# Kernel optimization log

Hardware: AMD Instinct MI355X
Metric: run time of the kernel (lower is better)

The kernel has to match this reference:

```python
import jax, jax.numpy as jnp
import numpy as np

# Model dims (from ModelArgs defaults)
B, S, DIM = 1, 1024, 2880
H, HKV, HD = 64, 8, 64        # query heads, kv heads, head dim
GROUP = H // HKV              # 8 query heads per kv head
WINDOW = 128                  # sliding window (layer_idx=0 -> active)
THETA = 150000.0


def setup_inputs() -> dict:
    key = jax.random.key(0)
    ks = jax.random.split(key, 10)
    rn = lambda k, shape, sc: (jax.random.normal(k, shape, jnp.float32) * sc)
    return {
        "x": rn(ks[0], (B, S, DIM), 1.0),
        "wq_w": rn(ks[1], (H * HD, DIM), 0.02),
        "wq_b": rn(ks[2], (H * HD,), 0.02),
        "wk_w": rn(ks[3], (HKV * HD, DIM), 0.02),
        "wk_b": rn(ks[4], (HKV * HD,), 0.02),
        "wv_w": rn(ks[5], (HKV * HD, DIM), 0.02),
        "wv_b": rn(ks[6], (HKV * HD,), 0.02),
        "wo_w": rn(ks[7], (DIM, H * HD), 0.02),
        "wo_b": rn(ks[8], (DIM,), 0.02),
        "sinks": rn(ks[9], (H,), 1.0),
    }


def _rope(t):
    # t: [B, S, h, HD]; half-split (rotate_half) RoPE with base THETA
    half = HD // 2
    inv_freq = 1.0 / (THETA ** (jnp.arange(half, dtype=jnp.float32) * 2.0 / HD))
    ang = jnp.arange(S, dtype=jnp.float32)[:, None] * inv_freq      # [S, half]
    cos = jnp.cos(ang)[None, :, None, :]
    sin = jnp.sin(ang)[None, :, None, :]
    t1, t2 = t[..., :half], t[..., half:]
    return jnp.concatenate([t1 * cos - t2 * sin, t1 * sin + t2 * cos], axis=-1)


def reference(x, wq_w, wq_b, wk_w, wk_b, wv_w, wv_b, wo_w, wo_b, sinks):
    # Projections (nn.Linear: y = x @ W^T + b)
    q = (jnp.einsum('bsd,ed->bse', x, wq_w) + wq_b).reshape(B, S, H, HD)
    k = (jnp.einsum('bsd,ed->bse', x, wk_w) + wk_b).reshape(B, S, HKV, HD)
    v = (jnp.einsum('bsd,ed->bse', x, wv_w) + wv_b).reshape(B, S, HKV, HD)

    q = _rope(q)
    k = _rope(k)

    # GQA: expand kv heads to match query heads
    k = jnp.repeat(k, GROUP, axis=2)   # [B, S, H, HD]
    v = jnp.repeat(v, GROUP, axis=2)

    scale = HD ** -0.5
    scores = jnp.einsum('bihd,bjhd->bhij', q, k) * scale   # [B, H, S, S]

    # Causal + sliding-window mask: attend to j with 0 <= i-j < WINDOW
    i = jnp.arange(S)[:, None]
    j = jnp.arange(S)[None, :]
    allowed = (j <= i) & ((i - j) < WINDOW)
    scores = jnp.where(allowed, scores, jnp.float32(-1e30))

    # Softmax with per-head learnable sink logit folded into normalization
    sink = sinks[None, :, None, None]                       # [1, H, 1, 1]
    m = jnp.maximum(jnp.max(scores, axis=-1, keepdims=True), sink)
    e = jnp.exp(scores - m)
    denom = jnp.sum(e, axis=-1, keepdims=True) + jnp.exp(sink - m)
    probs = e / denom                                       # sink mass dropped

    out = jnp.einsum('bhij,bjhd->bihd', probs, v).reshape(B, S, H * HD)
    return jnp.einsum('bse,de->bsd', out, wo_w) + wo_b
```

## Files before the change

kernel.cpp:

```cpp
#include <hip/hip_runtime.h>

typedef __attribute__((ext_vector_type(4))) float f32x4;
typedef __attribute__((ext_vector_type(8))) short s16x8;
typedef unsigned short u16;

#define DEVI __device__ __forceinline__

DEVI u16 f2bf(float f) {
    union { float f; unsigned int u; } v; v.f = f;
    unsigned int r = v.u + 0x7FFFu + ((v.u >> 16) & 1u);
    return (u16)(r >> 16);
}
DEVI float bf2f(u16 b) {
    union { unsigned int u; float f; } v; v.u = ((unsigned int)b) << 16;
    return v.f;
}

typedef __attribute__((address_space(1))) void gv_t;
typedef __attribute__((address_space(3))) void sv_t;

#define GLOAD16(SRC, DST) __builtin_amdgcn_global_load_lds( \
    (gv_t*)(SRC), (sv_t*)(DST), 16, 0, 0)

DEVI f32x4 mfma_bf16(s16x8 a, s16x8 b, f32x4 c) {
    return __builtin_amdgcn_mfma_f32_16x16x32_bf16(a, b, c, 0, 0, 0);
}

template<bool AF32>
__global__ __launch_bounds__(512, 4) void gemmrs(
    const void* __restrict__ Ap, int lda, int kit, int ntot,
    const float* __restrict__ W0, int t0, int n0, int c0,
    const float* __restrict__ W1, int t1, int n1, int c1,
    const float* __restrict__ W2, int t2, int n2, int c2,
    u16* __restrict__ C, int ldc, long long cstride)
{
    __shared__ u16 Als[2][128 * 64];
    __shared__ u16 Bls[2][128 * 64];

    const int lin = blockIdx.x;
    const int xc  = lin & 7;
    const int mm  = lin >> 3;
    const int nbl = xc + 8 * (mm >> 3);
    const int yt  = mm & 7;
    if (nbl >= ntot) return;

    const float* Af = (const float*)Ap;
    const u16*   Ab = (const u16*)Ap;

    const int tid  = threadIdx.x;
    const int lane = tid & 63;
    const int wid  = tid >> 6;
    const int li   = lane & 15;
    const int lg   = lane >> 4;
    const int m0   = yt * 128;

    const float* W; int nt0, nsz, cb;
    if (nbl < t0)           { W = W0; nt0 = nbl * 128;             nsz = n0; cb = c0; }
    else if (nbl < t0 + t1) { W = W1; nt0 = (nbl - t0) * 128;      nsz = n1; cb = c1; }
    else                    { W = W2; nt0 = (nbl - t0 - t1) * 128; nsz = n2; cb = c2; }

    const int z  = blockIdx.z;
    const int S  = gridDim.z;
    const int it0 = (z * kit) / S;
    const int it1 = ((z + 1) * kit) / S;
    u16* Cp = C + (long long)z * cstride;

    const int wm = (wid >> 2) * 64;
    const int wn = (wid & 3) * 32;

    const int srow = tid >> 3;
    const int c8   = tid & 7;
    const int sc   = c8 ^ (srow & 7);
    const int wrow0 = (nt0 + srow      > nsz - 1) ? nsz - 1 : nt0 + srow;
    const int wrow1 = (nt0 + srow + 64 > nsz - 1) ? nsz - 1 : nt0 + srow + 64;

    f32x4 acc[4][2];
    #pragma unroll
    for (int mi = 0; mi < 4; ++mi)
        #pragma unroll
        for (int ni = 0; ni < 2; ++ni)
            acc[mi][ni] = (f32x4){0.f, 0.f, 0.f, 0.f};

    f32x4 ra[2][2];
    s16x8 rab[2];
    f32x4 rw[2][2];

#define LOADT(TT)                                                               \
    do {                                                                        \
        int k0_ = (TT) * 64;                                                    \
        _Pragma("unroll")                                                       \
        for (int j = 0; j < 2; ++j) {                                           \
            int row_ = j * 64 + srow;                                           \
            if (AF32) {                                                         \
                const float* p_ = Af + (size_t)(m0 + row_) * lda + k0_ + c8 * 8;\
                ra[j][0] = *(const f32x4*)p_;                                   \
                ra[j][1] = *(const f32x4*)(p_ + 4);                             \
            } else {                                                            \
                rab[j] = *(const s16x8*)(Ab + (size_t)(m0 + row_) * lda + k0_ + c8 * 8); \
            }                                                                   \
            int wr_ = j ? wrow1 : wrow0;                                        \
            const float* q_ = W + (size_t)wr_ * lda + k0_ + c8 * 8;             \
            rw[j][0] = *(const f32x4*)q_;                                       \
            rw[j][1] = *(const f32x4*)(q_ + 4);                                 \
        }                                                                       \
    } while (0)

#define WRITET(BI)                                                              \
    do {                                                                        \
        _Pragma("unroll")                                                       \
        for (int j = 0; j < 2; ++j) {                                           \
            int row_ = j * 64 + srow;                                           \
            s16x8 va_;                                                          \
            if (AF32) {                                                         \
                _Pragma("unroll")                                               \
                for (int e = 0; e < 4; ++e) {                                   \
                    va_[e]     = (short)f2bf(ra[j][0][e]);                      \
                    va_[4 + e] = (short)f2bf(ra[j][1][e]);                      \
                }                                                               \
            } else {                                                            \
                va_ = rab[j];                                                   \
            }                                                                   \
            *(s16x8*)&Als[BI][row_ * 64 + sc * 8] = va_;                        \
            s16x8 vw_;                                                          \
            _Pragma("unroll")                                                   \
            for (int e = 0; e < 4; ++e) {                                       \
                vw_[e]     = (short)f2bf(rw[j][0][e]);                          \
                vw_[4 + e] = (short)f2bf(rw[j][1][e]);                          \
            }                                                                   \
            *(s16x8*)&Bls[BI][row_ * 64 + sc * 8] = vw_;                        \
        }                                                                       \
    } while (0)

    LOADT(it0);
    WRITET(0);
    __syncthreads();

    for (int t = it0; t < it1; ++t) {
        const int bi = (t - it0) & 1;

        if (t + 1 < it1) LOADT(t + 1);

        s16x8 bfv[2][2];
        #pragma unroll
        for (int ni = 0; ni < 2; ++ni)
            #pragma unroll
            for (int kc = 0; kc < 2; ++kc) {
                int row = wn + ni * 16 + li;
                int ch  = (kc * 4 + lg) ^ (row & 7);
                bfv[ni][kc] = *(const s16x8*)&Bls[bi][row * 64 + ch * 8];
            }
        #pragma unroll
        for (int mi = 0; mi < 4; ++mi) {
            s16x8 af[2];
            #pragma unroll
            for (int kc = 0; kc < 2; ++kc) {
                int row = wm + mi * 16 + li;
                int ch  = (kc * 4 + lg) ^ (row & 7);
                af[kc] = *(const s16x8*)&Als[bi][row * 64 + ch * 8];
            }
            #pragma unroll
            for (int ni = 0; ni < 2; ++ni)
                #pragma unroll
                for (int kc = 0; kc < 2; ++kc)
                    acc[mi][ni] = mfma_bf16(af[kc], bfv[ni][kc], acc[mi][ni]);
        }

        if (t + 1 < it1) WRITET(bi ^ 1);

        __syncthreads();
    }
#undef LOADT
#undef WRITET

    #pragma unroll
    for (int ni = 0; ni < 2; ++ni) {
        int colr = nt0 + wn + ni * 16 + li;
        if (colr < nsz) {
            #pragma unroll
            for (int mi = 0; mi < 4; ++mi)
                #pragma unroll
                for (int r = 0; r < 4; ++r) {
                    int row = m0 + wm + mi * 16 + lg * 4 + r;
                    Cp[(size_t)row * ldc + cb + colr] = f2bf(acc[mi][ni][r]);
                }
        }
    }
}

__global__ void rope_kernel(const u16* __restrict__ qkvp,
                            const float* __restrict__ qb, const float* __restrict__ kb,
                            const float* __restrict__ vb,
                            u16* __restrict__ qo, u16* __restrict__ ko, u16* __restrict__ vo)
{
    const long long PST = 1024LL * 5120;
    int id = blockIdx.x * 256 + threadIdx.x;
    int s  = id / 2560;
    int r  = id % 2560;
    const u16* r0 = qkvp + (size_t)s * 5120;
    if (r < 2304) {
        bool isq = r < 2048;
        int rr   = isq ? r : r - 2048;
        int hh   = rr >> 5;
        int d    = rr & 31;
        int col  = (isq ? 0 : 4096) + hh * 64 + d;
        int bcol = isq ? col : col - 4096;
        const float* bias = isq ? qb : kb;
        float t1 = bf2f(r0[col])      + bf2f(r0[col + PST])      + bf2f(r0[col + 2 * PST])      + bias[bcol];
        float t2 = bf2f(r0[col + 32]) + bf2f(r0[col + 32 + PST]) + bf2f(r0[col + 32 + 2 * PST]) + bias[bcol + 32];
        float ang = (float)s * exp2f((float)d * -0.5373314f);
        float sn, cs;
        sincosf(ang, &sn, &cs);
        float sc = isq ? 0.125f : 1.0f;
        float o1 = (t1 * cs - t2 * sn) * sc;
        float o2 = (t1 * sn + t2 * cs) * sc;
        u16* dst = isq ? qo : ko;
        int ldd  = isq ? 4096 : 512;
        dst[(size_t)s * ldd + bcol]      = f2bf(o1);
        dst[(size_t)s * ldd + bcol + 32] = f2bf(o2);
    } else {
        int e = (r - 2304) * 2;
        int c0 = 4608 + e;
        float v0 = bf2f(r0[c0])     + bf2f(r0[c0 + PST])     + bf2f(r0[c0 + 2 * PST])     + vb[e];
        float v1 = bf2f(r0[c0 + 1]) + bf2f(r0[c0 + 1 + PST]) + bf2f(r0[c0 + 1 + 2 * PST]) + vb[e + 1];
        vo[(size_t)s * 512 + e]     = f2bf(v0);
        vo[(size_t)s * 512 + e + 1] = f2bf(v1);
    }
}

__global__ void reduce_out_kernel(const u16* __restrict__ parts,
                                  const float* __restrict__ bias,
                                  float* __restrict__ out)
{
    int id = blockIdx.x * 256 + threadIdx.x;
    const long long stride = 1024LL * 2880;
    long long base = (long long)id * 8;
    float s[8];
    #pragma unroll
    for (int j = 0; j < 8; ++j) s[j] = 0.f;
    #pragma unroll
    for (int p = 0; p < 5; ++p) {
        s16x8 v = *(const s16x8*)(parts + p * stride + base);
        #pragma unroll
        for (int j = 0; j < 8; ++j) s[j] += bf2f((u16)v[j]);
    }
    int cb = (int)(base % 2880);
    f32x4 b0 = *(const f32x4*)(bias + cb);
    f32x4 b1 = *(const f32x4*)(bias + cb + 4);
    f32x4 o0 = {s[0] + b0[0], s[1] + b0[1], s[2] + b0[2], s[3] + b0[3]};
    f32x4 o1 = {s[4] + b1[0], s[5] + b1[1], s[6] + b1[2], s[7] + b1[3]};
    *(f32x4*)(out + base)     = o0;
    *(f32x4*)(out + base + 4) = o1;
}

__global__ __launch_bounds__(256, 2) void attn_kernel(
    const u16* __restrict__ Q, const u16* __restrict__ Kb, const u16* __restrict__ Vb,
    const float* __restrict__ sinks, u16* __restrict__ Ob)
{
    __shared__ u16 Kls[64 * 64];
    __shared__ u16 Pls[4][16 * 72];

    const int h    = blockIdx.x;
    const int qblk = blockIdx.y;
    const int kvh  = h >> 3;
    const int tid  = threadIdx.x;
    const int lane = tid & 63;
    const int w    = tid >> 6;
    const int li   = lane & 15;
    const int lg   = lane >> 4;
    const int qw   = qblk * 64 + w * 16;

    s16x8 aq[2];
    {
        const u16* qrow = Q + ((size_t)(qw + li) * 64 + h) * 64 + lg * 8;
        aq[0] = *(const s16x8*)(qrow);
        aq[1] = *(const s16x8*)(qrow + 32);
    }

    const float snk = sinks[h];
    float m_run[4], l_run[4];
    f32x4 oacc[4];
    #pragma unroll
    for (int r = 0; r < 4; ++r) { m_run[r] = snk; l_run[r] = 1.0f; }
    #pragma unroll
    for (int ni = 0; ni < 4; ++ni) oacc[ni] = (f32x4){0.f, 0.f, 0.f, 0.f};

    const int srow = tid >> 3;
    const int slc  = (tid & 7) ^ (srow & 7);

    for (int t = 0; t < 3; ++t) {
        int jt = qblk - 2 + t;
        if (jt < 0) continue;
        int j0 = jt * 64;

        #pragma unroll
        for (int it = 0; it < 2; ++it) {
            const u16* src = Kb + ((size_t)(j0 + it * 32 + srow) * 8 + kvh) * 64 + slc * 8;
            GLOAD16(src, &Kls[(it * 256 + w * 64) * 8]);
        }
        __syncthreads();

        f32x4 sc[4];
        #pragma unroll
        for (int nf = 0; nf < 4; ++nf) {
            sc[nf] = (f32x4){0.f, 0.f, 0.f, 0.f};
            #pragma unroll
            for (int kc = 0; kc < 2; ++kc) {
                int row = nf * 16 + li;
                int ch  = (kc * 4 + lg) ^ (row & 7);
                s16x8 bk = *(const s16x8*)&Kls[row * 64 + ch * 8];
                sc[nf] = mfma_bf16(aq[kc], bk, sc[nf]);
            }
        }

        #pragma unroll
        for (int r = 0; r < 4; ++r) {
            const int qg = qw + lg * 4 + r;
            float mx = -1e30f;
            #pragma unroll
            for (int nf = 0; nf < 4; ++nf) {
                int jg = j0 + nf * 16 + li;
                bool ok = (jg <= qg) && (qg - jg < 128);
                float v = ok ? sc[nf][r] : -1e30f;
                sc[nf][r] = v;
                mx = fmaxf(mx, v);
            }
            #pragma unroll
            for (int off = 1; off < 16; off <<= 1)
                mx = fmaxf(mx, __shfl_xor(mx, off));
            float mnew = fmaxf(m_run[r], mx);
            float corr = __expf(m_run[r] - mnew);
            m_run[r] = mnew;
            float rs = 0.f;
            #pragma unroll
            for (int nf = 0; nf < 4; ++nf) {
                float p = __expf(sc[nf][r] - mnew);
                rs += p;
                Pls[w][(lg * 4 + r) * 72 + nf * 16 + li] = f2bf(p);
            }
            #pragma unroll
            for (int off = 1; off < 16; off <<= 1)
                rs += __shfl_xor(rs, off);
            l_run[r] = l_run[r] * corr + rs;
            #pragma unroll
            for (int ni = 0; ni < 4; ++ni) oacc[ni][r] *= corr;
        }
        __syncthreads();

        #pragma unroll
        for (int kc = 0; kc < 2; ++kc) {
            s16x8 pa = *(const s16x8*)&Pls[w][li * 72 + kc * 32 + lg * 8];
            #pragma unroll
            for (int ni = 0; ni < 4; ++ni) {
                const u16* vsrc = Vb + ((size_t)(j0 + kc * 32 + lg * 8) * 8 + kvh) * 64 + ni * 16 + li;
                s16x8 bv;
                #pragma unroll
                for (int i = 0; i < 8; ++i) bv[i] = (short)vsrc[(size_t)i * 512];
                oacc[ni] = mfma_bf16(pa, bv, oacc[ni]);
            }
        }
    }

    #pragma unroll
    for (int r = 0; r < 4; ++r) {
        float inv = 1.0f / l_run[r];
        #pragma unroll
        for (int ni = 0; ni < 4; ++ni)
            Ob[((size_t)(qw + lg * 4 + r) * 64 + h) * 64 + ni * 16 + li] = f2bf(oacc[ni][r] * inv);
    }
}

extern "C" void kernel_launch(void* const* d_in, const int* in_sizes, int n_in,
                              void* d_out, int out_size, void* d_ws, size_t ws_size,
                              hipStream_t stream)
{
    const float* x     = (const float*)d_in[0];
    const float* wq_w  = (const float*)d_in[1];
    const float* wq_b  = (const float*)d_in[2];
    const float* wk_w  = (const float*)d_in[3];
    const float* wk_b  = (const float*)d_in[4];
    const float* wv_w  = (const float*)d_in[5];
    const float* wv_b  = (const float*)d_in[6];
    const float* wo_w  = (const float*)d_in[7];
    const float* wo_b  = (const float*)d_in[8];
    const float* sinks = (const float*)d_in[9];

    char* ws = (char*)d_ws;
    u16*   qkvp = (u16*)(ws + 35389440ULL);
    u16*   qr   = (u16*)(ws + 0);
    u16*   kr   = (u16*)(ws + 8388608ULL);
    u16*   vbf  = (u16*)(ws + 9437184ULL);
    u16*   attb = (u16*)(ws + 10485760ULL);
    u16*   oprt = (u16*)(ws + 58982400ULL);

    (void)in_sizes; (void)n_in; (void)out_size; (void)ws_size;

    gemmrs<true><<<dim3(320, 1, 3), 512, 0, stream>>>(x, 2880, 45, 40,
        wq_w, 32, 4096, 0,
        wk_w, 4, 512, 4096,
        wv_w, 4, 512, 4608,
        qkvp, 5120, 1024LL * 5120);
    rope_kernel<<<10240, 256, 0, stream>>>(qkvp, wq_b, wk_b, wv_b, qr, kr, vbf);
    attn_kernel<<<dim3(64, 16), 256, 0, stream>>>(qr, kr, vbf, sinks, attb);
    gemmrs<false><<<dim3(192, 1, 5), 512, 0, stream>>>(attb, 4096, 64, 23,
        wo_w, 23, 2880, 0,
        wo_w, 0, 0, 0,
        wo_w, 0, 0, 0,
        oprt, 2880, 1024LL * 2880);
    reduce_out_kernel<<<1440, 256, 0, stream>>>(oprt, wo_b, (float*)d_out);
}
```

Measured before the change: 141.1 us.

## Pre-convert x to bf16, load A tiles via global_load_lds, vectorize rope

```diff
diff --git a/kernel.cpp b/kernel.cpp
--- a/kernel.cpp
+++ b/kernel.cpp
@@ -26,9 +26,18 @@
     return __builtin_amdgcn_mfma_f32_16x16x32_bf16(a, b, c, 0, 0, 0);
 }
 
-template<bool AF32>
-__global__ __launch_bounds__(512, 4) void gemmrs(
-    const void* __restrict__ Ap, int lda, int kit, int ntot,
+__global__ void cvt_x_kernel(const float* __restrict__ x, u16* __restrict__ xb)
+{
+    int id = blockIdx.x * 256 + threadIdx.x;
+    f32x4 v = *(const f32x4*)(x + (size_t)id * 4);
+    union { u16 u[4]; unsigned long long ll; } o;
+    #pragma unroll
+    for (int j = 0; j < 4; ++j) o.u[j] = f2bf(v[j]);
+    *(unsigned long long*)(xb + (size_t)id * 4) = o.ll;
+}
+
+__global__ __launch_bounds__(512, 4) void gemmhy(
+    const u16* __restrict__ A, int lda, int kit, int ntot,
     const float* __restrict__ W0, int t0, int n0, int c0,
     const float* __restrict__ W1, int t1, int n1, int c1,
     const float* __restrict__ W2, int t2, int n2, int c2,
@@ -44,9 +53,6 @@
     const int yt  = mm & 7;
     if (nbl >= ntot) return;
 
-    const float* Af = (const float*)Ap;
-    const u16*   Ab = (const u16*)Ap;
-
     const int tid  = threadIdx.x;
     const int lane = tid & 63;
     const int wid  = tid >> 6;
@@ -68,12 +74,6 @@
     const int wm = (wid >> 2) * 64;
     const int wn = (wid & 3) * 32;
 
-    const int srow = tid >> 3;
-    const int c8   = tid & 7;
-    const int sc   = c8 ^ (srow & 7);
-    const int wrow0 = (nt0 + srow      > nsz - 1) ? nsz - 1 : nt0 + srow;
-    const int wrow1 = (nt0 + srow + 64 > nsz - 1) ? nsz - 1 : nt0 + srow + 64;
-
     f32x4 acc[4][2];
     #pragma unroll
     for (int mi = 0; mi < 4; ++mi)
@@ -81,64 +81,62 @@
         for (int ni = 0; ni < 2; ++ni)
             acc[mi][ni] = (f32x4){0.f, 0.f, 0.f, 0.f};
 
-    f32x4 ra[2][2];
-    s16x8 rab[2];
-    f32x4 rw[2][2];
-
-#define LOADT(TT)                                                               \
+    const int wrowl = tid >> 2;
+    const int c80   = (tid & 3) * 2;
+    const int wrowg = (nt0 + wrowl > nsz - 1) ? nsz - 1 : nt0 + wrowl;
+
+    f32x4 rw[4];
+
+#define LOADW(TT)                                                               \
+    do {                                                                        \
+        const float* q_ = W + (size_t)wrowg * lda + (TT) * 64 + c80 * 8;        \
+        rw[0] = *(const f32x4*)q_;                                              \
+        rw[1] = *(const f32x4*)(q_ + 4);                                        \
+        rw[2] = *(const f32x4*)(q_ + 8);                                        \
+        rw[3] = *(const f32x4*)(q_ + 12);                                       \
+    } while (0)
+
+#define GLOADA(TT, BI)                                                          \
     do {                                                                        \
         int k0_ = (TT) * 64;                                                    \
         _Pragma("unroll")                                                       \
         for (int j = 0; j < 2; ++j) {                                           \
-            int row_ = j * 64 + srow;                                           \
-            if (AF32) {                                                         \
-                const float* p_ = Af + (size_t)(m0 + row_) * lda + k0_ + c8 * 8;\
-                ra[j][0] = *(const f32x4*)p_;                                   \
-                ra[j][1] = *(const f32x4*)(p_ + 4);                             \
-            } else {                                                            \
-                rab[j] = *(const s16x8*)(Ab + (size_t)(m0 + row_) * lda + k0_ + c8 * 8); \
-            }                                                                   \
-            int wr_ = j ? wrow1 : wrow0;                                        \
-            const float* q_ = W + (size_t)wr_ * lda + k0_ + c8 * 8;             \
-            rw[j][0] = *(const f32x4*)q_;                                       \
-            rw[j][1] = *(const f32x4*)(q_ + 4);                                 \
+            int g_   = j * 512 + tid;                                           \
+            int row_ = g_ >> 3;                                                 \
+            int cs_  = (g_ & 7) ^ (row_ & 7);                                   \
+            GLOAD16(A + (size_t)(m0 + row_) * lda + k0_ + cs_ * 8,              \
+                    &Als[BI][g_ * 8]);                                          \
         }                                                                       \
     } while (0)
 
-#define WRITET(BI)                                                              \
+#define WRITEW(BI)                                                              \
     do {                                                                        \
+        s16x8 w0_, w1_;                                                         \
         _Pragma("unroll")                                                       \
-        for (int j = 0; j < 2; ++j) {                                           \
-            int row_ = j * 64 + srow;                                           \
-            s16x8 va_;                                                          \
-            if (AF32) {                                                         \
-                _Pragma("unroll")                                               \
-                for (int e = 0; e < 4; ++e) {                                   \
-                    va_[e]     = (short)f2bf(ra[j][0][e]);                      \
-                    va_[4 + e] = (short)f2bf(ra[j][1][e]);                      \
-                }                                                               \
-            } else {                                                            \
-                va_ = rab[j];                                                   \
-            }                                                                   \
-            *(s16x8*)&Als[BI][row_ * 64 + sc * 8] = va_;                        \
-            s16x8 vw_;                                                          \
-            _Pragma("unroll")                                                   \
-            for (int e = 0; e < 4; ++e) {                                       \
-                vw_[e]     = (short)f2bf(rw[j][0][e]);                          \
-                vw_[4 + e] = (short)f2bf(rw[j][1][e]);                          \
-            }                                                                   \
-            *(s16x8*)&Bls[BI][row_ * 64 + sc * 8] = vw_;                        \
+        for (int e = 0; e < 4; ++e) {                                           \
+            w0_[e]     = (short)f2bf(rw[0][e]);                                 \
+            w0_[4 + e] = (short)f2bf(rw[1][e]);                                 \
+            w1_[e]     = (short)f2bf(rw[2][e]);                                 \
+            w1_[4 + e] = (short)f2bf(rw[3][e]);                                 \
         }                                                                       \
+        int s0_ = c80 ^ (wrowl & 7);                                            \
+        int s1_ = (c80 + 1) ^ (wrowl & 7);                                      \
+        *(s16x8*)&Bls[BI][wrowl * 64 + s0_ * 8] = w0_;                          \
+        *(s16x8*)&Bls[BI][wrowl * 64 + s1_ * 8] = w1_;                          \
     } while (0)
 
-    LOADT(it0);
-    WRITET(0);
+    LOADW(it0);
+    GLOADA(it0, 0);
+    WRITEW(0);
     __syncthreads();
 
     for (int t = it0; t < it1; ++t) {
         const int bi = (t - it0) & 1;
 
-        if (t + 1 < it1) LOADT(t + 1);
+        if (t + 1 < it1) {
+            LOADW(t + 1);
+            GLOADA(t + 1, bi ^ 1);
+        }
 
         s16x8 bfv[2][2];
         #pragma unroll
@@ -165,12 +163,13 @@
                     acc[mi][ni] = mfma_bf16(af[kc], bfv[ni][kc], acc[mi][ni]);
         }
 
-        if (t + 1 < it1) WRITET(bi ^ 1);
+        if (t + 1 < it1) WRITEW(bi ^ 1);
 
         __syncthreads();
     }
-#undef LOADT
-#undef WRITET
+#undef LOADW
+#undef GLOADA
+#undef WRITEW
 
     #pragma unroll
     for (int ni = 0; ni < 2; ++ni) {
@@ -194,36 +193,63 @@
 {
     const long long PST = 1024LL * 5120;
     int id = blockIdx.x * 256 + threadIdx.x;
-    int s  = id / 2560;
-    int r  = id % 2560;
+    int s  = id / 352;
+    int g  = id % 352;
     const u16* r0 = qkvp + (size_t)s * 5120;
-    if (r < 2304) {
-        bool isq = r < 2048;
-        int rr   = isq ? r : r - 2048;
-        int hh   = rr >> 5;
-        int d    = rr & 31;
-        int col  = (isq ? 0 : 4096) + hh * 64 + d;
-        int bcol = isq ? col : col - 4096;
+
+    if (g < 288) {
+        bool isq = g < 256;
+        int gg   = isq ? g : g - 256;
+        int hh   = gg >> 2;
+        int dg   = gg & 3;
+        int col0 = (isq ? 0 : 4096) + hh * 64 + dg * 8;
+        int bcol = isq ? col0 : col0 - 4096;
         const float* bias = isq ? qb : kb;
-        float t1 = bf2f(r0[col])      + bf2f(r0[col + PST])      + bf2f(r0[col + 2 * PST])      + bias[bcol];
-        float t2 = bf2f(r0[col + 32]) + bf2f(r0[col + 32 + PST]) + bf2f(r0[col + 32 + 2 * PST]) + bias[bcol + 32];
-        float ang = (float)s * exp2f((float)d * -0.5373314f);
-        float sn, cs;
-        sincosf(ang, &sn, &cs);
+
+        float t1[8], t2[8];
+        #pragma unroll
+        for (int e = 0; e < 8; ++e) { t1[e] = bias[bcol + e]; t2[e] = bias[bcol + 32 + e]; }
+        #pragma unroll
+        for (int p = 0; p < 3; ++p) {
+            s16x8 lo = *(const s16x8*)(r0 + col0 + p * PST);
+            s16x8 hi = *(const s16x8*)(r0 + col0 + 32 + p * PST);
+            #pragma unroll
+            for (int e = 0; e < 8; ++e) {
+                t1[e] += bf2f((u16)lo[e]);
+                t2[e] += bf2f((u16)hi[e]);
+            }
+        }
         float sc = isq ? 0.125f : 1.0f;
-        float o1 = (t1 * cs - t2 * sn) * sc;
-        float o2 = (t1 * sn + t2 * cs) * sc;
+        s16x8 o1, o2;
+        #pragma unroll
+        for (int e = 0; e < 8; ++e) {
+            int d = dg * 8 + e;
+            float ang = (float)s * exp2f((float)d * -0.5373314f);
+            float sn, cs;
+            sincosf(ang, &sn, &cs);
+            o1[e] = (short)f2bf((t1[e] * cs - t2[e] * sn) * sc);
+            o2[e] = (short)f2bf((t1[e] * sn + t2[e] * cs) * sc);
+        }
         u16* dst = isq ? qo : ko;
         int ldd  = isq ? 4096 : 512;
-        dst[(size_t)s * ldd + bcol]      = f2bf(o1);
-        dst[(size_t)s * ldd + bcol + 32] = f2bf(o2);
+        *(s16x8*)(dst + (size_t)s * ldd + bcol)      = o1;
+        *(s16x8*)(dst + (size_t)s * ldd + bcol + 32) = o2;
     } else {
-        int e = (r - 2304) * 2;
-        int c0 = 4608 + e;
-        float v0 = bf2f(r0[c0])     + bf2f(r0[c0 + PST])     + bf2f(r0[c0 + 2 * PST])     + vb[e];
-        float v1 = bf2f(r0[c0 + 1]) + bf2f(r0[c0 + 1 + PST]) + bf2f(r0[c0 + 1 + 2 * PST]) + vb[e + 1];
-        vo[(size_t)s * 512 + e]     = f2bf(v0);
-        vo[(size_t)s * 512 + e + 1] = f2bf(v1);
+        int gg   = g - 288;
+        int col0 = 4608 + gg * 8;
+        float t[8];
+        #pragma unroll
+        for (int e = 0; e < 8; ++e) t[e] = vb[gg * 8 + e];
+        #pragma unroll
+        for (int p = 0; p < 3; ++p) {
+            s16x8 v = *(const s16x8*)(r0 + col0 + p * PST);
+            #pragma unroll
+            for (int e = 0; e < 8; ++e) t[e] += bf2f((u16)v[e]);
+        }
+        s16x8 o;
+        #pragma unroll
+        for (int e = 0; e < 8; ++e) o[e] = (short)f2bf(t[e]);
+        *(s16x8*)(vo + (size_t)s * 512 + gg * 8) = o;
     }
 }
 
@@ -385,6 +411,7 @@
     const float* sinks = (const float*)d_in[9];
 
     char* ws = (char*)d_ws;
+    u16*   xb   = (u16*)(ws + 0);
     u16*   qkvp = (u16*)(ws + 35389440ULL);
     u16*   qr   = (u16*)(ws + 0);
     u16*   kr   = (u16*)(ws + 8388608ULL);
@@ -394,14 +421,15 @@
 
     (void)in_sizes; (void)n_in; (void)out_size; (void)ws_size;
 
-    gemmrs<true><<<dim3(320, 1, 3), 512, 0, stream>>>(x, 2880, 45, 40,
+    cvt_x_kernel<<<2880, 256, 0, stream>>>(x, xb);
+    gemmhy<<<dim3(320, 1, 3), 512, 0, stream>>>(xb, 2880, 45, 40,
         wq_w, 32, 4096, 0,
         wk_w, 4, 512, 4096,
         wv_w, 4, 512, 4608,
         qkvp, 5120, 1024LL * 5120);
-    rope_kernel<<<10240, 256, 0, stream>>>(qkvp, wq_b, wk_b, wv_b, qr, kr, vbf);
+    rope_kernel<<<1408, 256, 0, stream>>>(qkvp, wq_b, wk_b, wv_b, qr, kr, vbf);
     attn_kernel<<<dim3(64, 16), 256, 0, stream>>>(qr, kr, vbf, sinks, attb);
-    gemmrs<false><<<dim3(192, 1, 5), 512, 0, stream>>>(attb, 4096, 64, 23,
+    gemmhy<<<dim3(192, 1, 5), 512, 0, stream>>>(attb, 4096, 64, 23,
         wo_w, 23, 2880, 0,
         wo_w, 0, 0, 0,
         wo_w, 0, 0, 0,
```

Result: no change. 139.4 us (-1.2%).
